# Kernel tuning notes

Measured on AMD Instinct MI355X. Metric: run time of the kernel, lower is better.

The kernel has to match this reference:

```python
import jax, jax.numpy as jnp
import numpy as np

N, E, KS, DIM = 6890, 41340, 5, 2
K = KS * KS  # 25 spline kernel buckets


def spline_conv(x, edge_index, pseudo, weight, root, bias):
    """Degree-1 open B-spline conv (SplineGCN), mean aggregation + root + bias.
    x: [N, Fin], weight: [K, Fin, Fout], root: [Fin, Fout], bias: [Fout]."""
    row, col = edge_index[0], edge_index[1]  # target, source
    pos = pseudo * (KS - 1)                   # [E, 2] in [0, KS-1]
    i0 = jnp.clip(jnp.floor(pos), 0, KS - 2).astype(jnp.int32)  # [E, 2]
    frac = pos - i0                           # [E, 2]
    # 4 nonzero basis products per edge (2 per dim)
    off = jnp.array([[0, 0], [1, 0], [0, 1], [1, 1]], dtype=jnp.int32)  # [4, 2]
    b_dim = jnp.stack([1.0 - frac, frac], axis=-1)  # [E, 2, 2] (dim, which-knot)
    w = b_dim[:, 0, off[:, 0]] * b_dim[:, 1, off[:, 1]]       # [E, 4]
    idx = (i0[:, None, 0] + off[None, :, 0]) + KS * (i0[:, None, 1] + off[None, :, 1])  # [E, 4]
    # transform all nodes by all K kernels once: [N, K, Fout]
    xw = jnp.einsum('ni,kio->nko', x, weight)
    g = xw[col[:, None], idx]                 # [E, 4, Fout] gather
    msg = jnp.einsum('es,eso->eo', w, g)      # [E, Fout]
    agg = jax.ops.segment_sum(msg, row, num_segments=N)
    deg = jax.ops.segment_sum(jnp.ones((E,), x.dtype), row, num_segments=N)
    agg = agg / jnp.maximum(deg, 1.0)[:, None]
    return agg + x @ root + bias


def setup_inputs() -> dict:
    key = jax.random.key(0)
    ks = jax.random.split(key, 20)
    def gl(k, shape):  # glorot-ish
        fan = shape[-2] if len(shape) > 1 else shape[-1]
        return jax.random.normal(k, shape, jnp.float32) / np.sqrt(fan)
    inp = {
        'x': jax.random.normal(ks[0], (N, 544), jnp.float32),
        'edge_index': jax.random.randint(ks[1], (2, E), 0, N),
        'pseudo': jax.random.uniform(ks[2], (E, DIM), jnp.float32),
        'W_lin': gl(ks[3], (544, 16)), 'b_lin': jnp.zeros((16,), jnp.float32),
        'w1': gl(ks[4], (K, 16, 32)),  'r1': gl(ks[5], (16, 32)),  'bi1': jnp.zeros((32,), jnp.float32),
        'w2': gl(ks[6], (K, 32, 64)),  'r2': gl(ks[7], (32, 64)),  'bi2': jnp.zeros((64,), jnp.float32),
        'w3': gl(ks[8], (K, 64, 128)), 'r3': gl(ks[9], (64, 128)), 'bi3': jnp.zeros((128,), jnp.float32),
        'W1': gl(ks[10], (128, 256)), 'b1': jnp.zeros((256,), jnp.float32),
        'W2': gl(ks[11], (256, 6890)), 'b2': jnp.zeros((6890,), jnp.float32),
    }
    return inp


def reference(x, edge_index, pseudo, W_lin, b_lin, w1, r1, bi1, w2, r2, bi2, w3, r3, bi3, W1, b1, W2, b2):
    h = jax.nn.elu(x @ W_lin + b_lin)
    h = jax.nn.elu(spline_conv(h, edge_index, pseudo, w1, r1, bi1))
    h = jax.nn.elu(spline_conv(h, edge_index, pseudo, w2, r2, bi2))
    h = jax.nn.elu(spline_conv(h, edge_index, pseudo, w3, r3, bi3))
    h = jax.nn.elu(h @ W1 + b1)
    # dropout is identity in eval mode
    logits = h @ W2 + b2
    return jax.nn.log_softmax(logits, axis=-1)
```

## Files before the change

### kernel.cpp

```cpp
#include <hip/hip_runtime.h>
#include <hip/hip_bf16.h>

#define NND 6890
#define NED 41340

typedef __bf16 bf16x8 __attribute__((ext_vector_type(8)));
typedef float f32x4 __attribute__((ext_vector_type(4)));
typedef unsigned short u16x4 __attribute__((ext_vector_type(4)));
typedef unsigned short u16x8 __attribute__((ext_vector_type(8)));

__device__ inline unsigned short f32_bf16(float f) {
  unsigned int u = __float_as_uint(f);
  unsigned int r = (u + 0x7FFFu + ((u >> 16) & 1u)) >> 16;
  return (unsigned short)r;
}
__device__ inline void split2(float v, unsigned short& hi, unsigned short& lo) {
  unsigned short h = f32_bf16(v);
  float hf = __uint_as_float((unsigned int)h << 16);
  hi = h;
  lo = f32_bf16(v - hf);
}
__device__ inline float elu_f(float v) { return v > 0.f ? v : (expf(v) - 1.f); }

__device__ __forceinline__ void gload_lds16(const void* g, void* l) {
  __builtin_amdgcn_global_load_lds((const __attribute__((address_space(1))) void*)g,
                                   (__attribute__((address_space(3))) void*)l, 16, 0, 0);
}

__global__ void zero_int_kernel(int* p, int n) {
  int i = blockIdx.x * blockDim.x + threadIdx.x;
  if (i < n) p[i] = 0;
}

__global__ void edge_prep_kernel(const int* __restrict__ erow, const float* __restrict__ pseudo,
                                 float* __restrict__ ew, int* __restrict__ ek,
                                 int* __restrict__ deg, int E) {
  int e = blockIdx.x * blockDim.x + threadIdx.x;
  if (e >= E) return;
  float p0 = pseudo[2 * e + 0] * 4.0f;
  float p1 = pseudo[2 * e + 1] * 4.0f;
  int i0 = (int)floorf(p0); i0 = i0 < 0 ? 0 : (i0 > 3 ? 3 : i0);
  int i1 = (int)floorf(p1); i1 = i1 < 0 ? 0 : (i1 > 3 ? 3 : i1);
  float f0 = p0 - (float)i0, f1 = p1 - (float)i1;
  ew[4 * e + 0] = (1.f - f0) * (1.f - f1);
  ew[4 * e + 1] = f0 * (1.f - f1);
  ew[4 * e + 2] = (1.f - f0) * f1;
  ew[4 * e + 3] = f0 * f1;
  int b = i0 + 5 * i1;
  ek[4 * e + 0] = b; ek[4 * e + 1] = b + 1; ek[4 * e + 2] = b + 5; ek[4 * e + 3] = b + 6;
  atomicAdd(&deg[erow[e]], 1);
}

__global__ void scan_kernel(const int* __restrict__ deg, int* __restrict__ rowptr,
                            int* __restrict__ cursor, float* __restrict__ deginv, int n) {
  __shared__ int part[1024];
  int t = threadIdx.x;
  int CH = (n + 1023) >> 10;
  int base = t * CH;
  int s = 0;
  for (int j = 0; j < CH; ++j) { int i = base + j; if (i < n) s += deg[i]; }
  part[t] = s;
  __syncthreads();
  for (int off = 1; off < 1024; off <<= 1) {
    int v = (t >= off) ? part[t - off] : 0;
    __syncthreads();
    part[t] += v;
    __syncthreads();
  }
  int run = (t == 0) ? 0 : part[t - 1];
  for (int j = 0; j < CH; ++j) {
    int i = base + j;
    if (i < n) {
      rowptr[i] = run; cursor[i] = run;
      int d = deg[i];
      deginv[i] = 1.0f / fmaxf((float)d, 1.0f);
      run += d;
    }
  }
  if (t == 1023) rowptr[n] = part[1023];
}

__global__ void csr_fill_kernel(const int* __restrict__ erow, int* __restrict__ cursor,
                                int* __restrict__ csr, int E) {
  int e = blockIdx.x * blockDim.x + threadIdx.x;
  if (e >= E) return;
  int slot = atomicAdd(&cursor[erow[e]], 1);
  csr[slot] = e;
}

__global__ void b_build_kernel(const float* __restrict__ x, const int* __restrict__ ecol,
                               const float* __restrict__ ew, const int* __restrict__ ek,
                               const int* __restrict__ rowptr, const int* __restrict__ csr,
                               const float* __restrict__ deginv,
                               float* __restrict__ B, int Fin) {
  extern __shared__ float lds[];
  int r = blockIdx.x;
  int T = blockDim.x;
  int tid = threadIdx.x;
  int nb = 25 * Fin;
  for (int j = tid; j < nb; j += T) lds[j] = 0.f;
  if (tid < Fin) lds[nb + tid] = x[(size_t)r * Fin + tid];
  __syncthreads();
  int p0 = rowptr[r], p1 = rowptr[r + 1];
  int s = tid / Fin;
  int i = tid - s * Fin;
  for (int p = p0; p < p1; ++p) {
    int e = csr[p];
    int c = ecol[e];
    float wv = ew[4 * e + s];
    int k = ek[4 * e + s];
    float xv = x[(size_t)c * Fin + i];
    lds[k * Fin + i] += wv * xv;
    __syncthreads();
  }
  float dinv = deginv[r];
  int tot = nb + Fin;
  for (int j = tid; j < tot; j += T) {
    float v = lds[j];
    if (j < nb) v *= dinv;
    B[(size_t)r * tot + j] = v;
  }
}

__global__ void weights_prep_kernel(const float* __restrict__ W_lin, const float* __restrict__ w1,
                                    const float* __restrict__ r1, const float* __restrict__ w2,
                                    const float* __restrict__ r2, const float* __restrict__ w3,
                                    const float* __restrict__ r3, const float* __restrict__ W1,
                                    unsigned short* __restrict__ Th, unsigned short* __restrict__ Tl) {
  const int tstart[9] = {0, 17, 30, 31, 81, 83, 283, 291, 323};
  const int jK[8]    = {544, 400, 16, 800, 32, 1600, 64, 128};
  const int jF[8]    = {16, 32, 32, 64, 64, 128, 128, 256};
  const int jldt[8]  = {544, 416, 416, 832, 832, 1664, 1664, 128};
  const int jkoff[8] = {0, 0, 400, 0, 800, 0, 1600, 0};
  const int jdst[8]  = {0, 8704, 8704, 22016, 22016, 75264, 75264, 288256};
  int b = blockIdx.x;
  int job = 0;
  while (job < 7 && b >= tstart[job + 1]) ++job;
  int t = b - tstart[job];
  int fxc = (jF[job] + 31) >> 5;
  int kt = t / fxc, ft = t % fxc;
  const float* src;
  switch (job) {
    case 0: src = W_lin; break;
    case 1: src = w1; break;
    case 2: src = r1; break;
    case 3: src = w2; break;
    case 4: src = r2; break;
    case 5: src = w3; break;
    case 6: src = r3; break;
    default: src = W1; break;
  }
  int K = jK[job], F = jF[job], ldt = jldt[job], koff = jkoff[job];
  unsigned short* th = Th + jdst[job];
  unsigned short* tl = Tl + jdst[job];
  int k0 = kt * 32, c0 = ft * 32;
  __shared__ float tbuf[32][33];
  int tx = threadIdx.x & 31, ty = threadIdx.x >> 5;
  for (int j = ty; j < 32; j += 8) {
    int gk = k0 + j, gc = c0 + tx;
    tbuf[j][tx] = (gk < K && gc < F) ? src[(size_t)gk * F + gc] : 0.f;
  }
  __syncthreads();
  for (int j = ty; j < 32; j += 8) {
    int gc = c0 + j, gk = k0 + tx;
    if (gc < F && gk < K) {
      unsigned short h, lo2;
      split2(tbuf[tx][j], h, lo2);
      th[(size_t)gc * ldt + koff + gk] = h;
      tl[(size_t)gc * ldt + koff + gk] = lo2;
    }
  }
}

template <int BN>
__global__ __launch_bounds__(256) void gemm_x3_partial_kernel(
    const float* __restrict__ A, const unsigned short* __restrict__ Wth,
    const unsigned short* __restrict__ Wtl, float* __restrict__ P,
    int M, int Kd, int F, int KS) {
  constexpr int BK = 32;
  constexpr int NF = BN / 16;
  constexpr int WU = (BK * BN) / 4;
  constexpr int WREP = (WU + 255) / 256;
  __shared__ __align__(16) unsigned short Ah[2][64][40];
  __shared__ __align__(16) unsigned short Al[2][64][40];
  __shared__ __align__(16) unsigned short Wh[2][BN][40];
  __shared__ __align__(16) unsigned short Wl[2][BN][40];
  int tid = threadIdx.x;
  int wave = tid >> 6, lane = tid & 63;
  int g = lane >> 4, r = lane & 15;
  int row0 = blockIdx.y * 64;
  int col0 = blockIdx.x * BN;
  int z = blockIdx.z;
  int nt = Kd >> 5;
  int ta = z * nt / KS, tb = (z + 1) * nt / KS;

  f32x4 acc[NF];
#pragma unroll
  for (int n = 0; n < NF; ++n)
#pragma unroll
    for (int q = 0; q < 4; ++q) acc[n][q] = 0.f;

  f32x4 ra[2];
  u16x4 rwh[WREP], rwl[WREP];

  auto loadTiles = [&](int kb) {
#pragma unroll
    for (int rep = 0; rep < 2; ++rep) {
      int u = tid + rep * 256;
      int rr = u >> 3, kq = (u & 7) * 4;
      int gr = row0 + rr;
      f32x4 v = {0.f, 0.f, 0.f, 0.f};
      if (gr < M) v = *(const f32x4*)(A + (size_t)gr * Kd + kb + kq);
      ra[rep] = v;
    }
#pragma unroll
    for (int rep = 0; rep < WREP; ++rep) {
      int u = tid + rep * 256;
      if (u < WU) {
        int cc = u >> 3, kq = (u & 7) * 4;
        rwh[rep] = *(const u16x4*)(Wth + (size_t)(col0 + cc) * Kd + kb + kq);
        rwl[rep] = *(const u16x4*)(Wtl + (size_t)(col0 + cc) * Kd + kb + kq);
      }
    }
  };
  auto writeLDS = [&](int buf) {
#pragma unroll
    for (int rep = 0; rep < 2; ++rep) {
      int u = tid + rep * 256;
      int rr = u >> 3, kq = (u & 7) * 4;
      u16x4 h, l;
#pragma unroll
      for (int j = 0; j < 4; ++j) {
        unsigned short hh, ll;
        split2(ra[rep][j], hh, ll);
        h[j] = hh; l[j] = ll;
      }
      *(u16x4*)&Ah[buf][rr][kq] = h;
      *(u16x4*)&Al[buf][rr][kq] = l;
    }
#pragma unroll
    for (int rep = 0; rep < WREP; ++rep) {
      int u = tid + rep * 256;
      if (u < WU) {
        int cc = u >> 3, kq = (u & 7) * 4;
        *(u16x4*)&Wh[buf][cc][kq] = rwh[rep];
        *(u16x4*)&Wl[buf][cc][kq] = rwl[rep];
      }
    }
  };

  int n = tb - ta;
  loadTiles(ta * BK);
  writeLDS(0);
  __syncthreads();
  for (int tt = 0; tt < n; ++tt) {
    int cur = tt & 1;
    if (tt + 1 < n) loadTiles((ta + tt + 1) * BK);
    bf16x8 fah = *(const bf16x8*)&Ah[cur][wave * 16 + r][g * 8];
    bf16x8 fal = *(const bf16x8*)&Al[cur][wave * 16 + r][g * 8];
#pragma unroll
    for (int nn = 0; nn < NF; ++nn) {
      bf16x8 fbh = *(const bf16x8*)&Wh[cur][nn * 16 + r][g * 8];
      bf16x8 fbl = *(const bf16x8*)&Wl[cur][nn * 16 + r][g * 8];
      acc[nn] = __builtin_amdgcn_mfma_f32_16x16x32_bf16(fah, fbh, acc[nn], 0, 0, 0);
      acc[nn] = __builtin_amdgcn_mfma_f32_16x16x32_bf16(fal, fbh, acc[nn], 0, 0, 0);
      acc[nn] = __builtin_amdgcn_mfma_f32_16x16x32_bf16(fah, fbl, acc[nn], 0, 0, 0);
    }
    if (tt + 1 < n) writeLDS(cur ^ 1);
    __syncthreads();
  }
#pragma unroll
  for (int nn = 0; nn < NF; ++nn) {
    int gc = col0 + nn * 16 + r;
#pragma unroll
    for (int q = 0; q < 4; ++q) {
      int gr = row0 + wave * 16 + g * 4 + q;
      if (gr < M) P[((size_t)z * M + gr) * F + gc] = acc[nn][q];
    }
  }
}

__global__ __launch_bounds__(256) void combine_elu_kernel(
    const float* __restrict__ P, const float* __restrict__ bias,
    float* __restrict__ outF, unsigned short* __restrict__ outB,
    int M, int F, int KS) {
  int i4 = blockIdx.x * 256 + threadIdx.x;
  int fv = F >> 2;
  int total = M * fv;
  if (i4 >= total) return;
  int gr = i4 / fv, c4 = (i4 - gr * fv) * 4;
  f32x4 s = {0.f, 0.f, 0.f, 0.f};
  for (int z = 0; z < KS; ++z)
    s += *(const f32x4*)(P + ((size_t)z * M + gr) * F + c4);
  f32x4 bv = *(const f32x4*)(bias + c4);
#pragma unroll
  for (int j = 0; j < 4; ++j) s[j] = elu_f(s[j] + bv[j]);
  if (outB) {
    u16x4 o;
#pragma unroll
    for (int j = 0; j < 4; ++j) o[j] = f32_bf16(s[j]);
    *(u16x4*)(outB + (size_t)gr * F + c4) = o;
  } else {
    *(f32x4*)(outF + (size_t)gr * F + c4) = s;
  }
}

__global__ void w2_cast_transpose_kernel(const float* __restrict__ W2,
                                         unsigned short* __restrict__ Wt, int K, int N) {
  __shared__ float t[32][33];
  int c0 = blockIdx.x * 32, k0 = blockIdx.y * 32;
  int tx = threadIdx.x, ty = threadIdx.y;
  for (int j = ty; j < 32; j += 8) {
    int gk = k0 + j, gc = c0 + tx;
    t[j][tx] = (gk < K && gc < N) ? W2[(size_t)gk * N + gc] : 0.f;
  }
  __syncthreads();
  for (int j = ty; j < 32; j += 8) {
    int gc = c0 + j, gk = k0 + tx;
    if (gc < N && gk < K) Wt[(size_t)gc * K + gk] = f32_bf16(t[tx][j]);
  }
}

__global__ __launch_bounds__(256) void gemm_final_kernel(
    const unsigned short* __restrict__ A, const unsigned short* __restrict__ Bt,
    const float* __restrict__ bias, float* __restrict__ C, int M, int N) {
  __shared__ __align__(16) unsigned short lds[2][64][256];
  int tid = threadIdx.x;
  int w = tid >> 6, l = tid & 63;
  int row0 = blockIdx.y * 64, col0 = blockIdx.x * 64;
  {
    int half = l >> 5;
    int c = l & 31;
#pragma unroll
    for (int i = 0; i < 8; ++i) {
      int rb = w * 16 + i * 2;
      int rr = rb + half;
      int gra = row0 + rr; if (gra >= M) gra = M - 1;
      int grb = col0 + rr; if (grb >= N) grb = N - 1;
      int cs = ((c ^ (rr & 7)) << 3);
      gload_lds16(A + (size_t)gra * 256 + cs, &lds[0][rb][0]);
      gload_lds16(Bt + (size_t)grb * 256 + cs, &lds[1][rb][0]);
    }
  }
  __syncthreads();
  int wm = w >> 1, wn = w & 1;
  int g = l >> 4, r = l & 15;
  int rs = r & 7;
  f32x4 acc[2][2];
#pragma unroll
  for (int mi = 0; mi < 2; ++mi)
#pragma unroll
    for (int ni = 0; ni < 2; ++ni)
#pragma unroll
      for (int q = 0; q < 4; ++q) acc[mi][ni][q] = 0.f;
#pragma unroll
  for (int t = 0; t < 8; ++t) {
    int ck = ((4 * t + g) ^ rs) << 3;
    bf16x8 fa[2], fb[2];
#pragma unroll
    for (int mi = 0; mi < 2; ++mi)
      fa[mi] = *(const bf16x8*)&lds[0][wm * 32 + mi * 16 + r][ck];
#pragma unroll
    for (int ni = 0; ni < 2; ++ni)
      fb[ni] = *(const bf16x8*)&lds[1][wn * 32 + ni * 16 + r][ck];
#pragma unroll
    for (int mi = 0; mi < 2; ++mi)
#pragma unroll
      for (int ni = 0; ni < 2; ++ni)
        acc[mi][ni] = __builtin_amdgcn_mfma_f32_16x16x32_bf16(fb[ni], fa[mi], acc[mi][ni], 0, 0, 0);
  }
#pragma unroll
  for (int mi = 0; mi < 2; ++mi) {
    int gr = row0 + wm * 32 + mi * 16 + r;
    if (gr >= M) continue;
    float* crow = C + (size_t)gr * N;
#pragma unroll
    for (int ni = 0; ni < 2; ++ni) {
      int gc0 = col0 + wn * 32 + ni * 16 + g * 4;
      f32x4 v = acc[mi][ni];
      if (gc0 + 4 <= N) {
        f32x4 bv = *(const f32x4*)(bias + gc0);
        v += bv;
        *(f32x4*)(crow + gc0) = v;
      } else {
#pragma unroll
        for (int q = 0; q < 4; ++q)
          if (gc0 + q < N) crow[gc0 + q] = v[q] + bias[gc0 + q];
      }
    }
  }
}

__global__ __launch_bounds__(256) void log_softmax_kernel(float* __restrict__ out, int N) {
  extern __shared__ float row[];
  __shared__ float wred[4];
  const int NV = 1722;
  float* p = out + (size_t)blockIdx.x * N;
  int tid = threadIdx.x;
  float m = -1e30f;
  for (int c = tid; c < NV; c += 256) {
    f32x4 v = *(const f32x4*)(p + 4 * c);
    *(f32x4*)&row[4 * c] = v;
    m = fmaxf(fmaxf(fmaxf(v[0], v[1]), fmaxf(v[2], v[3])), m);
  }
  if (tid < 2) { float v = p[6888 + tid]; row[6888 + tid] = v; m = fmaxf(m, v); }
  for (int off = 32; off; off >>= 1) m = fmaxf(m, __shfl_xor(m, off));
  if ((tid & 63) == 0) wred[tid >> 6] = m;
  __syncthreads();
  m = fmaxf(fmaxf(wred[0], wred[1]), fmaxf(wred[2], wred[3]));
  float s = 0.f;
  for (int c = tid; c < NV; c += 256) {
    f32x4 v = *(const f32x4*)&row[4 * c];
    s += expf(v[0] - m) + expf(v[1] - m) + expf(v[2] - m) + expf(v[3] - m);
  }
  if (tid < 2) s += expf(row[6888 + tid] - m);
  for (int off = 32; off; off >>= 1) s += __shfl_xor(s, off);
  __syncthreads();
  if ((tid & 63) == 0) wred[tid >> 6] = s;
  __syncthreads();
  float lse = m + logf(wred[0] + wred[1] + wred[2] + wred[3]);
  for (int c = tid; c < NV; c += 256) {
    f32x4 v = *(const f32x4*)&row[4 * c];
#pragma unroll
    for (int j = 0; j < 4; ++j) v[j] -= lse;
    *(f32x4*)(p + 4 * c) = v;
  }
  if (tid < 2) p[6888 + tid] = row[6888 + tid] - lse;
}

extern "C" void kernel_launch(void* const* d_in, const int* in_sizes, int n_in,
                              void* d_out, int out_size, void* d_ws, size_t ws_size,
                              hipStream_t stream) {
  const int N = NND, E = NED;
  const float* x      = (const float*)d_in[0];
  const int*   ei     = (const int*)d_in[1];
  const float* pseudo = (const float*)d_in[2];
  const float* W_lin  = (const float*)d_in[3];
  const float* b_lin  = (const float*)d_in[4];
  const float* w1  = (const float*)d_in[5];
  const float* r1  = (const float*)d_in[6];
  const float* bi1 = (const float*)d_in[7];
  const float* w2  = (const float*)d_in[8];
  const float* r2  = (const float*)d_in[9];
  const float* bi2 = (const float*)d_in[10];
  const float* w3  = (const float*)d_in[11];
  const float* r3  = (const float*)d_in[12];
  const float* bi3 = (const float*)d_in[13];
  const float* W1  = (const float*)d_in[14];
  const float* b1  = (const float*)d_in[15];
  const float* W2  = (const float*)d_in[16];
  const float* b2  = (const float*)d_in[17];
  const int* erow = ei;
  const int* ecol = ei + E;

  char* scratch = (char*)d_out;
  size_t off = 0;
  auto alloc = [&](size_t bytes) -> void* {
    void* p = scratch + off;
    off = (off + bytes + 255) & ~(size_t)255;
    return p;
  };
  float* Bbuf   = (float*)alloc((size_t)N * 1664 * 4);
  float* h0     = (float*)alloc((size_t)N * 16 * 4);
  float* h1     = (float*)alloc((size_t)N * 32 * 4);
  float* h2     = (float*)alloc((size_t)N * 64 * 4);
  float* h3     = (float*)alloc((size_t)N * 128 * 4);
  unsigned short* Wth = (unsigned short*)alloc((size_t)321024 * 2);
  unsigned short* Wtl = (unsigned short*)alloc((size_t)321024 * 2);
  float* Pbuf   = (float*)alloc((size_t)4 * N * 128 * 4);
  float* ew     = (float*)alloc((size_t)E * 4 * 4);
  int*   ek     = (int*)alloc((size_t)E * 4 * 4);
  int*   deg    = (int*)alloc((size_t)N * 4);
  float* deginv = (float*)alloc((size_t)N * 4);
  int*   rowptr = (int*)alloc((size_t)(N + 1) * 4);
  int*   cursor = (int*)alloc((size_t)N * 4);
  int*   csr    = (int*)alloc((size_t)E * 4);

  unsigned short* h4b = (unsigned short*)d_ws;
  unsigned short* W2t = (unsigned short*)((char*)d_ws + (size_t)N * 256 * 2);

  zero_int_kernel<<<(N + 255) / 256, 256, 0, stream>>>(deg, N);
  edge_prep_kernel<<<(E + 255) / 256, 256, 0, stream>>>(erow, pseudo, ew, ek, deg, E);
  scan_kernel<<<1, 1024, 0, stream>>>(deg, rowptr, cursor, deginv, N);
  csr_fill_kernel<<<(E + 255) / 256, 256, 0, stream>>>(erow, cursor, csr, E);

  weights_prep_kernel<<<323, 256, 0, stream>>>(W_lin, w1, r1, w2, r2, w3, r3, W1, Wth, Wtl);

  auto cgrid = [](int M_, int F_) { return dim3((M_ * (F_ / 4) + 255) / 256); };

  gemm_x3_partial_kernel<16><<<dim3(1, 108, 4), 256, 0, stream>>>(x, Wth + 0, Wtl + 0, Pbuf, N, 544, 16, 4);
  combine_elu_kernel<<<cgrid(N, 16), 256, 0, stream>>>(Pbuf, b_lin, h0, nullptr, N, 16, 4);

  b_build_kernel<<<N, 64, 26 * 16 * 4, stream>>>(h0, ecol, ew, ek, rowptr, csr, deginv, Bbuf, 16);
  gemm_x3_partial_kernel<32><<<dim3(1, 108, 4), 256, 0, stream>>>(Bbuf, Wth + 8704, Wtl + 8704, Pbuf, N, 416, 32, 4);
  combine_elu_kernel<<<cgrid(N, 32), 256, 0, stream>>>(Pbuf, bi1, h1, nullptr, N, 32, 4);

  b_build_kernel<<<N, 128, 26 * 32 * 4, stream>>>(h1, ecol, ew, ek, rowptr, csr, deginv, Bbuf, 32);
  gemm_x3_partial_kernel<64><<<dim3(1, 108, 4), 256, 0, stream>>>(Bbuf, Wth + 22016, Wtl + 22016, Pbuf, N, 832, 64, 4);
  combine_elu_kernel<<<cgrid(N, 64), 256, 0, stream>>>(Pbuf, bi2, h2, nullptr, N, 64, 4);

  b_build_kernel<<<N, 256, 26 * 64 * 4, stream>>>(h2, ecol, ew, ek, rowptr, csr, deginv, Bbuf, 64);
  gemm_x3_partial_kernel<128><<<dim3(1, 108, 4), 256, 0, stream>>>(Bbuf, Wth + 75264, Wtl + 75264, Pbuf, N, 1664, 128, 4);
  combine_elu_kernel<<<cgrid(N, 128), 256, 0, stream>>>(Pbuf, bi3, h3, nullptr, N, 128, 4);

  gemm_x3_partial_kernel<128><<<dim3(2, 108, 2), 256, 0, stream>>>(h3, Wth + 288256, Wtl + 288256, Pbuf, N, 128, 256, 2);
  combine_elu_kernel<<<cgrid(N, 256), 256, 0, stream>>>(Pbuf, b1, nullptr, h4b, N, 256, 2);

  w2_cast_transpose_kernel<<<dim3(216, 8), dim3(32, 8), 0, stream>>>(W2, W2t, 256, N);

  gemm_final_kernel<<<dim3(108, 108), 256, 0, stream>>>(h4b, W2t, b2, (float*)d_out, N, N);

  log_softmax_kernel<<<N, 256, (size_t)N * 4, stream>>>((float*)d_out, N);

  (void)in_sizes; (void)n_in; (void)out_size; (void)ws_size;
}
```

Measured before the change: 305.3 us.

## Fuse log-softmax into final GEMM via two-pass recompute, use LDS atomics in B-build

The final GEMM now runs twice. The first pass emits per-row, per-tile online-softmax (max, sum) statistics; a small kernel reduces them to a per-row log-sum-exp; the second pass recomputes the GEMM and writes logits minus that value directly. This removes the separate log_softmax kernel's full read and rewrite of the large N×N output, at the cost of doubling the GEMM compute. Separately, b_build accumulates with LDS atomicAdd instead of a block barrier per edge, cutting synchronisation per edge.

New measurement: 492.7 us. +61.4%, slower.

```diff
diff --git a/kernel.cpp b/kernel.cpp
--- a/kernel.cpp
+++ b/kernel.cpp
@@ -110,9 +110,9 @@
     float wv = ew[4 * e + s];
     int k = ek[4 * e + s];
     float xv = x[(size_t)c * Fin + i];
-    lds[k * Fin + i] += wv * xv;
-    __syncthreads();
-  }
+    atomicAdd(&lds[k * Fin + i], wv * xv);
+  }
+  __syncthreads();
   float dinv = deginv[r];
   int tot = nb + Fin;
   for (int j = tid; j < tot; j += T) {
@@ -321,9 +321,11 @@
   }
 }
 
+template <int MODE>
 __global__ __launch_bounds__(256) void gemm_final_kernel(
     const unsigned short* __restrict__ A, const unsigned short* __restrict__ Bt,
-    const float* __restrict__ bias, float* __restrict__ C, int M, int N) {
+    const float* __restrict__ bias, const float* __restrict__ lse,
+    float* __restrict__ outp, int M, int N) {
   __shared__ __align__(16) unsigned short lds[2][64][256];
   int tid = threadIdx.x;
   int w = tid >> 6, l = tid & 63;
@@ -369,63 +371,83 @@
       for (int ni = 0; ni < 2; ++ni)
         acc[mi][ni] = __builtin_amdgcn_mfma_f32_16x16x32_bf16(fb[ni], fa[mi], acc[mi][ni], 0, 0, 0);
   }
-#pragma unroll
-  for (int mi = 0; mi < 2; ++mi) {
-    int gr = row0 + wm * 32 + mi * 16 + r;
-    if (gr >= M) continue;
-    float* crow = C + (size_t)gr * N;
-#pragma unroll
-    for (int ni = 0; ni < 2; ++ni) {
-      int gc0 = col0 + wn * 32 + ni * 16 + g * 4;
-      f32x4 v = acc[mi][ni];
-      if (gc0 + 4 <= N) {
-        f32x4 bv = *(const f32x4*)(bias + gc0);
-        v += bv;
-        *(f32x4*)(crow + gc0) = v;
-      } else {
+  if (MODE == 0) {
+#pragma unroll
+    for (int mi = 0; mi < 2; ++mi) {
+      int gr = row0 + wm * 32 + mi * 16 + r;
+      float vv[2][4];
+      float mloc = -3e38f;
+#pragma unroll
+      for (int ni = 0; ni < 2; ++ni) {
+        int gc0 = col0 + wn * 32 + ni * 16 + g * 4;
+#pragma unroll
+        for (int q = 0; q < 4; ++q) {
+          int gc = gc0 + q;
+          float v = (gc < N) ? (acc[mi][ni][q] + bias[gc]) : -3e38f;
+          vv[ni][q] = v;
+          mloc = fmaxf(mloc, v);
+        }
+      }
+      float sloc = 0.f;
+#pragma unroll
+      for (int ni = 0; ni < 2; ++ni) {
+        int gc0 = col0 + wn * 32 + ni * 16 + g * 4;
 #pragma unroll
         for (int q = 0; q < 4; ++q)
-          if (gc0 + q < N) crow[gc0 + q] = v[q] + bias[gc0 + q];
-      }
-    }
-  }
-}
-
-__global__ __launch_bounds__(256) void log_softmax_kernel(float* __restrict__ out, int N) {
-  extern __shared__ float row[];
-  __shared__ float wred[4];
-  const int NV = 1722;
-  float* p = out + (size_t)blockIdx.x * N;
-  int tid = threadIdx.x;
-  float m = -1e30f;
-  for (int c = tid; c < NV; c += 256) {
-    f32x4 v = *(const f32x4*)(p + 4 * c);
-    *(f32x4*)&row[4 * c] = v;
-    m = fmaxf(fmaxf(fmaxf(v[0], v[1]), fmaxf(v[2], v[3])), m);
-  }
-  if (tid < 2) { float v = p[6888 + tid]; row[6888 + tid] = v; m = fmaxf(m, v); }
-  for (int off = 32; off; off >>= 1) m = fmaxf(m, __shfl_xor(m, off));
-  if ((tid & 63) == 0) wred[tid >> 6] = m;
-  __syncthreads();
-  m = fmaxf(fmaxf(wred[0], wred[1]), fmaxf(wred[2], wred[3]));
-  float s = 0.f;
-  for (int c = tid; c < NV; c += 256) {
-    f32x4 v = *(const f32x4*)&row[4 * c];
-    s += expf(v[0] - m) + expf(v[1] - m) + expf(v[2] - m) + expf(v[3] - m);
-  }
-  if (tid < 2) s += expf(row[6888 + tid] - m);
-  for (int off = 32; off; off >>= 1) s += __shfl_xor(s, off);
-  __syncthreads();
-  if ((tid & 63) == 0) wred[tid >> 6] = s;
-  __syncthreads();
-  float lse = m + logf(wred[0] + wred[1] + wred[2] + wred[3]);
-  for (int c = tid; c < NV; c += 256) {
-    f32x4 v = *(const f32x4*)&row[4 * c];
-#pragma unroll
-    for (int j = 0; j < 4; ++j) v[j] -= lse;
-    *(f32x4*)(p + 4 * c) = v;
-  }
-  if (tid < 2) p[6888 + tid] = row[6888 + tid] - lse;
+          if (gc0 + q < N) sloc += expf(vv[ni][q] - mloc);
+      }
+#pragma unroll
+      for (int off = 16; off < 64; off <<= 1) {
+        float mo = __shfl_xor(mloc, off);
+        float so = __shfl_xor(sloc, off);
+        float mn = fmaxf(mloc, mo);
+        sloc = sloc * expf(mloc - mn) + so * expf(mo - mn);
+        mloc = mn;
+      }
+      if (g == 0 && gr < M) {
+        int hb = blockIdx.x * 2 + wn;
+        float2* sp = (float2*)(outp + 2 * ((size_t)hb * M + gr));
+        *sp = make_float2(mloc, sloc);
+      }
+    }
+  } else {
+#pragma unroll
+    for (int mi = 0; mi < 2; ++mi) {
+      int gr = row0 + wm * 32 + mi * 16 + r;
+      if (gr >= M) continue;
+      float L = lse[gr];
+      float* crow = outp + (size_t)gr * N;
+#pragma unroll
+      for (int ni = 0; ni < 2; ++ni) {
+        int gc0 = col0 + wn * 32 + ni * 16 + g * 4;
+        f32x4 v = acc[mi][ni];
+        if (gc0 + 4 <= N) {
+          f32x4 bv = *(const f32x4*)(bias + gc0);
+#pragma unroll
+          for (int q = 0; q < 4; ++q) v[q] = v[q] + bv[q] - L;
+          *(f32x4*)(crow + gc0) = v;
+        } else {
+#pragma unroll
+          for (int q = 0; q < 4; ++q)
+            if (gc0 + q < N) crow[gc0 + q] = v[q] + bias[gc0 + q] - L;
+        }
+      }
+    }
+  }
+}
+
+__global__ __launch_bounds__(256) void lse_kernel(const float* __restrict__ stats,
+                                                  float* __restrict__ lse, int M, int NH) {
+  int row = blockIdx.x * 256 + threadIdx.x;
+  if (row >= M) return;
+  float m = -3e38f, s = 0.f;
+  for (int hb = 0; hb < NH; ++hb) {
+    float2 v = *(const float2*)(stats + 2 * ((size_t)hb * M + row));
+    float mn = fmaxf(m, v.x);
+    s = s * expf(m - mn) + v.y * expf(v.x - mn);
+    m = mn;
+  }
+  lse[row] = m + logf(s);
 }
 
 extern "C" void kernel_launch(void* const* d_in, const int* in_sizes, int n_in,
@@ -468,6 +490,7 @@
   unsigned short* Wth = (unsigned short*)alloc((size_t)321024 * 2);
   unsigned short* Wtl = (unsigned short*)alloc((size_t)321024 * 2);
   float* Pbuf   = (float*)alloc((size_t)4 * N * 128 * 4);
+  float* stats  = (float*)alloc((size_t)216 * N * 2 * 4);
   float* ew     = (float*)alloc((size_t)E * 4 * 4);
   int*   ek     = (int*)alloc((size_t)E * 4 * 4);
   int*   deg    = (int*)alloc((size_t)N * 4);
@@ -478,6 +501,7 @@
 
   unsigned short* h4b = (unsigned short*)d_ws;
   unsigned short* W2t = (unsigned short*)((char*)d_ws + (size_t)N * 256 * 2);
+  float* lse = (float*)((char*)d_ws + (size_t)N * 256 * 4);
 
   zero_int_kernel<<<(N + 255) / 256, 256, 0, stream>>>(deg, N);
   edge_prep_kernel<<<(E + 255) / 256, 256, 0, stream>>>(erow, pseudo, ew, ek, deg, E);
@@ -508,9 +532,11 @@
 
   w2_cast_transpose_kernel<<<dim3(216, 8), dim3(32, 8), 0, stream>>>(W2, W2t, 256, N);
 
-  gemm_final_kernel<<<dim3(108, 108), 256, 0, stream>>>(h4b, W2t, b2, (float*)d_out, N, N);
-
-  log_softmax_kernel<<<N, 256, (size_t)N * 4, stream>>>((float*)d_out, N);
+  gemm_final_kernel<0><<<dim3(108, 108), 256, 0, stream>>>(h4b, W2t, b2, nullptr, stats, N, N);
+
+  lse_kernel<<<(N + 255) / 256, 256, 0, stream>>>(stats, lse, N, 216);
+
+  gemm_final_kernel<1><<<dim3(108, 108), 256, 0, stream>>>(h4b, W2t, b2, lse, (float*)d_out, N, N);
 
   (void)in_sizes; (void)n_in; (void)out_size; (void)ws_size;
 }
```
